# Optimization experiments

Measured on AMD Instinct MI355X. Metric: run time of the kernel, lower is better.

The kernel has to match this reference:

```python
import jax, jax.numpy as jnp
import numpy as np

B, T, V, E, U = 8192, 1, 4000, 256, 256
IN = E + E  # GRU input dim: concat(features[B,1,256], embedded tokens[B,1,256]) -> 512


def setup_inputs() -> dict:
    key = jax.random.key(0)
    ks = jax.random.split(key, 8)
    s = 0.05
    return {
        "tokens": jax.random.randint(ks[0], (B, T), 0, V),
        "features": jax.random.normal(ks[1], (B, E), jnp.float32),
        "hidden": jnp.zeros((B, U), jnp.float32),  # unused by the original call (gru gets no initial_state)
        "emb": jax.random.normal(ks[2], (V, E), jnp.float32) * s,
        "gru_kernel": jax.random.normal(ks[3], (IN, 3 * U), jnp.float32) * s,
        "gru_rkernel": jax.random.normal(ks[4], (U, 3 * U), jnp.float32) * s,
        "gru_bias": jnp.zeros((2, 3 * U), jnp.float32),  # reset_after=True: separate input/recurrent biases
        "fc1_w": jax.random.normal(ks[5], (U, U), jnp.float32) * s,
        "fc1_b": jnp.zeros((U,), jnp.float32),
        "fc2_w": jax.random.normal(ks[6], (U, V), jnp.float32) * s,
        "fc2_b": jnp.zeros((V,), jnp.float32),
    }


def reference(tokens, features, hidden, emb, gru_kernel, gru_rkernel, gru_bias,
              fc1_w, fc1_b, fc2_w, fc2_b):
    # Embedding lookup: [B,T,E]
    x = emb[tokens]
    # concat context vector on feature axis (forces T==1): [B,1,E+E]
    x = jnp.concatenate([features[:, None, :], x], axis=-1)
    # Keras GRU called without initial_state -> zeros initial state.
    h0 = jnp.zeros((x.shape[0], U), x.dtype)

    def step(h, xt):  # xt: [B, IN]; Keras GRU v3 (reset_after=True) cell; dropout off at inference
        gx = xt @ gru_kernel + gru_bias[0]      # [B, 3U]
        gh = h @ gru_rkernel + gru_bias[1]      # [B, 3U]
        xz, xr, xn = jnp.split(gx, 3, axis=-1)
        hz, hr, hn = jnp.split(gh, 3, axis=-1)
        z = jax.nn.sigmoid(xz + hz)
        r = jax.nn.sigmoid(xr + hr)
        n = jnp.tanh(xn + r * hn)
        h_new = z * h + (1.0 - z) * n
        return h_new, h_new

    state, seq = jax.lax.scan(step, h0, jnp.swapaxes(x, 0, 1))  # seq: [T,B,U]
    out = jnp.swapaxes(seq, 0, 1)               # [B,T,U]
    y = out @ fc1_w + fc1_b                     # [B,T,U]
    y = y.reshape(-1, y.shape[-1])              # [B*T, U]
    logits = y @ fc2_w + fc2_b                  # [B*T, V]
    return (logits, state)
```

## Files before the change

kernel.cpp:

```cpp
#include <hip/hip_runtime.h>
#include <stdint.h>

typedef unsigned short u16;
typedef __attribute__((ext_vector_type(8))) short bf16x8;
typedef __attribute__((ext_vector_type(4))) float f32x4;

#define Bsz   8192
#define Vv    4000
#define Vpad  4096
#define Ee    256
#define Uu    256
#define INd   512
#define G3    768

__device__ __forceinline__ u16 f2bf(float f) {
    union { float f; uint32_t i; } v; v.f = f;
    uint32_t x = v.i;
    return (u16)((x + 0x7fffu + ((x >> 16) & 1u)) >> 16);
}

__device__ __forceinline__ void gload16(const u16* g, u16* l) {
    __builtin_amdgcn_global_load_lds(
        (const __attribute__((address_space(1))) unsigned int*)g,
        (__attribute__((address_space(3))) unsigned int*)l, 16, 0, 0);
}

__global__ __launch_bounds__(256) void prep_all(
    const float* __restrict__ w1,  u16* __restrict__ w1t,
    const float* __restrict__ fc1, u16* __restrict__ fc1c,
    const float* __restrict__ fc2, u16* __restrict__ fc2t,
    const float* __restrict__ fc1b, const float* __restrict__ fc2b,
    float* __restrict__ bfused)
{
    __shared__ float t[32][33];
    __shared__ float red[4][64];
    int b = blockIdx.x;
    if (b >= 1472) {
        int nl = (b - 1472) * 64 + (threadIdx.x & 63);
        int kq = threadIdx.x >> 6;
        float s = 0.f;
        if (nl < Vv) {
            #pragma unroll 8
            for (int k = 0; k < 64; k++) {
                int kk = kq * 64 + k;
                s += fc1b[kk] * fc2[(size_t)kk * Vv + nl];
            }
        }
        red[kq][threadIdx.x & 63] = s;
        __syncthreads();
        if (kq == 0 && nl < Vv)
            bfused[nl] = red[0][nl & 63] + red[1][nl & 63] + red[2][nl & 63]
                       + red[3][nl & 63] + fc2b[nl];
        return;
    }
    if (b >= 384 && b < 448) {
        int i = (b - 384) * 1024 + threadIdx.x * 4;
        float4 v = *(const float4*)(fc1 + i);
        __align__(8) u16 o[4] = {f2bf(v.x), f2bf(v.y), f2bf(v.z), f2bf(v.w)};
        *(uint2*)&fc1c[i] = *(const uint2*)o;
        return;
    }
    const float* in; u16* out; int K, N, bx, by;
    if (b < 384) { in = w1;  out = w1t;  K = 512; N = 768; bx = b % 24;  by = b / 24; }
    else { b -= 448; in = fc2; out = fc2t; K = 256; N = Vv; bx = b % 128; by = b / 128; }
    int n0 = bx * 32, k0 = by * 32;
    int c = threadIdx.x & 31, r = threadIdx.x >> 5;
    int n = n0 + c;
    #pragma unroll
    for (int i = 0; i < 32; i += 8)
        t[r + i][c] = (n < N) ? in[(size_t)(k0 + r + i) * N + n] : 0.f;
    __syncthreads();
    #pragma unroll
    for (int i = 0; i < 32; i += 8)
        out[(size_t)(n0 + r + i) * K + k0 + c] = f2bf(t[c][r + i]);
}

__global__ __launch_bounds__(256) void gru_fused(
    const int* __restrict__ tokens, const float* __restrict__ features,
    const float* __restrict__ emb,  const u16* __restrict__ BT,
    const float* __restrict__ gb,
    u16* __restrict__ h,
    float* __restrict__ state)
{
    __shared__ __align__(16) u16 As[2][64 * 32];
    __shared__ __align__(16) u16 Bs[2][3][64 * 32];
    __shared__ int tok[64];

    int tid = threadIdx.x;
    int id  = blockIdx.y * gridDim.x + blockIdx.x;
    int sid = (id & 7) * 64 + (id >> 3);
    int m0  = (sid >> 2) * 64;
    int n0  = (sid & 3) * 64;
    if (tid < 64) tok[tid] = tokens[m0 + tid];

    int wid = tid >> 6, lane = tid & 63, quad = lane >> 4, l16 = lane & 15;
    int wm = wid * 16;

    f32x4 acc[3][4] = {};

    int r  = tid >> 2;
    int kc = (tid & 3) * 8;
    const u16* bg = BT + (size_t)(n0 + r) * INd + kc;
    const float* fsrc = features + (size_t)(m0 + r) * Ee + kc;

    #pragma unroll
    for (int g = 0; g < 3; g++)
        gload16(bg + (size_t)g * 256 * INd, &Bs[0][g][tid * 8]);
    float4 a = *(const float4*)fsrc;
    float4 c = *(const float4*)(fsrc + 4);
    {
        u16 o[8] = {f2bf(a.x), f2bf(a.y), f2bf(a.z), f2bf(a.w),
                    f2bf(c.x), f2bf(c.y), f2bf(c.z), f2bf(c.w)};
        *(uint4*)&As[0][tid * 8] = *(const uint4*)o;
    }
    a = *(const float4*)(fsrc + 32);
    c = *(const float4*)(fsrc + 36);

    int cur = 0;
    for (int k0 = 0; k0 < INd; k0 += 32) {
        __syncthreads();
        int k1 = k0 + 32;
        if (k1 < INd) {
            #pragma unroll
            for (int g = 0; g < 3; g++)
                gload16(bg + (size_t)g * 256 * INd + k1, &Bs[cur ^ 1][g][tid * 8]);
            u16 o[8] = {f2bf(a.x), f2bf(a.y), f2bf(a.z), f2bf(a.w),
                        f2bf(c.x), f2bf(c.y), f2bf(c.z), f2bf(c.w)};
            *(uint4*)&As[cur ^ 1][tid * 8] = *(const uint4*)o;
            int k2 = k0 + 64;
            if (k2 < INd) {
                const float* src = (k2 < Ee) ? (fsrc + k2)
                                 : (emb + (size_t)tok[r] * Ee + (k2 - Ee) + kc);
                a = *(const float4*)src;
                c = *(const float4*)(src + 4);
            }
        }
        bf16x8 af = *(const bf16x8*)&As[cur][(wm + l16) * 32 + quad * 8];
        #pragma unroll
        for (int g = 0; g < 3; g++)
            #pragma unroll
            for (int j = 0; j < 4; j++) {
                bf16x8 bfv = *(const bf16x8*)&Bs[cur][g][(j * 16 + l16) * 32 + quad * 8];
                acc[g][j] = __builtin_amdgcn_mfma_f32_16x16x32_bf16(af, bfv, acc[g][j], 0, 0, 0);
            }
        cur ^= 1;
    }

    #pragma unroll
    for (int j = 0; j < 4; j++) {
        int jj = n0 + j * 16 + l16;
        float bz  = gb[jj]          + gb[G3 + jj];
        float br  = gb[Uu + jj]     + gb[G3 + Uu + jj];
        float b0n = gb[2 * Uu + jj];
        float b1n = gb[G3 + 2 * Uu + jj];
        #pragma unroll
        for (int rr = 0; rr < 4; rr++) {
            int b = m0 + wm + quad * 4 + rr;
            float z  = 1.f / (1.f + __expf(-(acc[0][j][rr] + bz)));
            float rg = 1.f / (1.f + __expf(-(acc[1][j][rr] + br)));
            float n  = tanhf(acc[2][j][rr] + b0n + rg * b1n);
            float hv = (1.f - z) * n;
            h[(size_t)b * Uu + jj] = f2bf(hv);
            state[(size_t)b * Uu + jj] = hv;
        }
    }
}

template<int BMt, int BNt, bool OUT_BF16, bool HAS_BIAS>
__global__ __launch_bounds__(256) void gemm_bt(
    const u16* __restrict__ A, const u16* __restrict__ BT,
    const float* __restrict__ bias, void* __restrict__ Cout,
    int N, int K)
{
    constexpr int NW_N  = (BNt == 128) ? 2 : 1;
    constexpr int NW_M  = 4 / NW_N;
    constexpr int WROWS = BMt / NW_M;
    constexpr int MI    = WROWS / 16;

    __shared__ __align__(16) u16 As[2][BMt * 32];
    __shared__ __align__(16) u16 Bs[2][BNt * 32];

    int tid = threadIdx.x;
    int m0   = blockIdx.y * BMt;
    int n0   = blockIdx.x * BNt;
    int wid  = tid >> 6, lane = tid & 63, quad = lane >> 4, l16 = lane & 15;
    int wm   = (wid / NW_N) * WROWS;
    int wn   = (wid % NW_N) * 64;

    f32x4 acc[MI][4] = {};

    const u16* ag = A  + (size_t)(m0 + (tid >> 2)) * K + (tid & 3) * 8;
    const u16* bg = BT + (size_t)(n0 + (tid >> 2)) * K + (tid & 3) * 8;

    #pragma unroll
    for (int s = 0; s < BMt / 64; s++)
        gload16(ag + (size_t)s * 64 * K, &As[0][tid * 8 + s * 64 * 32]);
    #pragma unroll
    for (int s = 0; s < BNt / 64; s++)
        gload16(bg + (size_t)s * 64 * K, &Bs[0][tid * 8 + s * 64 * 32]);

    int cur = 0;
    for (int k0 = 0; k0 < K; k0 += 32) {
        __syncthreads();
        int k1 = k0 + 32;
        if (k1 < K) {
            #pragma unroll
            for (int s = 0; s < BMt / 64; s++)
                gload16(ag + (size_t)s * 64 * K + k1, &As[cur ^ 1][tid * 8 + s * 64 * 32]);
            #pragma unroll
            for (int s = 0; s < BNt / 64; s++)
                gload16(bg + (size_t)s * 64 * K + k1, &Bs[cur ^ 1][tid * 8 + s * 64 * 32]);
        }

        bf16x8 af[MI], bf[4];
        #pragma unroll
        for (int i = 0; i < MI; i++)
            af[i] = *(const bf16x8*)&As[cur][(wm + i * 16 + l16) * 32 + quad * 8];
        #pragma unroll
        for (int j = 0; j < 4; j++)
            bf[j] = *(const bf16x8*)&Bs[cur][(wn + j * 16 + l16) * 32 + quad * 8];
        #pragma unroll
        for (int i = 0; i < MI; i++)
            #pragma unroll
            for (int j = 0; j < 4; j++)
                acc[i][j] = __builtin_amdgcn_mfma_f32_16x16x32_bf16(af[i], bf[j], acc[i][j], 0, 0, 0);
        cur ^= 1;
    }

    #pragma unroll
    for (int i = 0; i < MI; i++)
    #pragma unroll
    for (int j = 0; j < 4; j++) {
        int gn = n0 + wn + j * 16 + l16;
        if (gn >= N) continue;
        float bv = HAS_BIAS ? bias[gn] : 0.f;
        #pragma unroll
        for (int r = 0; r < 4; r++) {
            int gm = m0 + wm + i * 16 + quad * 4 + r;
            float v = acc[i][j][r] + bv;
            if (OUT_BF16) ((u16*)Cout)[(size_t)gm * N + gn] = f2bf(v);
            else          ((float*)Cout)[(size_t)gm * N + gn] = v;
        }
    }
}

extern "C" void kernel_launch(void* const* d_in, const int* in_sizes, int n_in,
                              void* d_out, int out_size, void* d_ws, size_t ws_size,
                              hipStream_t stream)
{
    const int*   tokens   = (const int*)d_in[0];
    const float* features = (const float*)d_in[1];
    const float* emb      = (const float*)d_in[3];
    const float* w1       = (const float*)d_in[4];
    const float* gbias    = (const float*)d_in[6];
    const float* fc1w     = (const float*)d_in[7];
    const float* fc1b     = (const float*)d_in[8];
    const float* fc2w     = (const float*)d_in[9];
    const float* fc2b     = (const float*)d_in[10];

    float* logits = (float*)d_out;
    float* state  = logits + (size_t)Bsz * Vv;

    char* ws = (char*)d_ws;
    u16*   w1t    = (u16*)(ws);
    u16*   fc1c   = (u16*)(ws +   786432);
    u16*   fc2t   = (u16*)(ws +   917504);
    u16*   Wt     = (u16*)(ws +  3014656);
    u16*   h      = (u16*)(ws +  5111808);
    float* bfused = (float*)(ws + 9306112);

    prep_all<<<dim3(1536), 256, 0, stream>>>(w1, w1t, fc1w, fc1c, fc2w, fc2t,
                                             fc1b, fc2b, bfused);

    gemm_bt<64, 64, true, false><<<dim3(Uu / 64, Vpad / 64), 256, 0, stream>>>(
        fc2t, fc1c, nullptr, (void*)Wt, Uu, Uu);

    gru_fused<<<dim3(Uu / 64, Bsz / 64), 256, 0, stream>>>(
        tokens, features, emb, w1t, gbias, h, state);

    gemm_bt<128, 128, false, true><<<dim3(Vpad / 128, Bsz / 128), 256, 0, stream>>>(
        h, Wt, bfused, (void*)logits, Vv, Uu);
}
```

Measured before the change: 220.0 us.

## Merge GRU, fused-weight GEMM and bias prep into one launch

The separate prep, Wt-GEMM and GRU kernels are folded into one multi-role kernel whose block ranges run the GRU GEMM, the fc2·fc1 product, or the fused-bias reduction concurrently. The Wt product now reads fc1/fc2 in fp32 directly and converts to bf16 while staging, so the fc1 copy and fc2 transpose buffers go away. The intent is fewer launches, less intermediate global traffic, and overlap of independent work. The cost is a Wt GEMM with strided, uncoalesced fc2 loads and no async copy, plus a shared-memory footprint sized for the largest role.

Measured after the change: 211.4 us. 1.04x faster.

```diff
diff --git a/kernel.cpp b/kernel.cpp
--- a/kernel.cpp
+++ b/kernel.cpp
@@ -25,19 +25,180 @@
         (__attribute__((address_space(3))) unsigned int*)l, 16, 0, 0);
 }
 
-__global__ __launch_bounds__(256) void prep_all(
-    const float* __restrict__ w1,  u16* __restrict__ w1t,
-    const float* __restrict__ fc1, u16* __restrict__ fc1c,
-    const float* __restrict__ fc2, u16* __restrict__ fc2t,
+__global__ __launch_bounds__(256) void prep_w1(
+    const float* __restrict__ w1, u16* __restrict__ w1t)
+{
+    __shared__ float t[32][33];
+    int b  = blockIdx.x;
+    int bx = b % 24, by = b / 24;
+    int n0 = bx * 32, k0 = by * 32;
+    int c = threadIdx.x & 31, r = threadIdx.x >> 5;
+    #pragma unroll
+    for (int i = 0; i < 32; i += 8)
+        t[r + i][c] = w1[(size_t)(k0 + r + i) * 768 + n0 + c];
+    __syncthreads();
+    #pragma unroll
+    for (int i = 0; i < 32; i += 8)
+        w1t[(size_t)(n0 + r + i) * 512 + k0 + c] = f2bf(t[c][r + i]);
+}
+
+__global__ __launch_bounds__(256) void mid_all(
+    const int* __restrict__ tokens, const float* __restrict__ features,
+    const float* __restrict__ emb,  const u16* __restrict__ BT,
+    const float* __restrict__ gb,
+    u16* __restrict__ h,
+    float* __restrict__ state,
+    const float* __restrict__ fc2,
+    const float* __restrict__ fc1,
     const float* __restrict__ fc1b, const float* __restrict__ fc2b,
+    u16* __restrict__ Wt,
     float* __restrict__ bfused)
 {
-    __shared__ float t[32][33];
-    __shared__ float red[4][64];
-    int b = blockIdx.x;
-    if (b >= 1472) {
-        int nl = (b - 1472) * 64 + (threadIdx.x & 63);
-        int kq = threadIdx.x >> 6;
+    __shared__ __align__(16) char smem[33024];
+    int b   = blockIdx.x;
+    int tid = threadIdx.x;
+
+    if (b < 512) {
+        u16* AsP = (u16*)smem;
+        u16* BsP = AsP + 4096;
+        int* tok = (int*)(smem + 32768);
+
+        int sid = (b & 7) * 64 + (b >> 3);
+        int m0  = (sid >> 2) * 64;
+        int n0  = (sid & 3) * 64;
+        if (tid < 64) tok[tid] = tokens[m0 + tid];
+
+        int wid = tid >> 6, lane = tid & 63, quad = lane >> 4, l16 = lane & 15;
+        int wm = wid * 16;
+
+        f32x4 acc[3][4] = {};
+
+        int r  = tid >> 2;
+        int kc = (tid & 3) * 8;
+        const u16* bg = BT + (size_t)(n0 + r) * INd + kc;
+        const float* fsrc = features + (size_t)(m0 + r) * Ee + kc;
+
+        #pragma unroll
+        for (int g = 0; g < 3; g++)
+            gload16(bg + (size_t)g * 256 * INd, &BsP[g * 2048 + tid * 8]);
+        float4 a = *(const float4*)fsrc;
+        float4 c = *(const float4*)(fsrc + 4);
+        {
+            u16 o[8] = {f2bf(a.x), f2bf(a.y), f2bf(a.z), f2bf(a.w),
+                        f2bf(c.x), f2bf(c.y), f2bf(c.z), f2bf(c.w)};
+            *(uint4*)&AsP[tid * 8] = *(const uint4*)o;
+        }
+        a = *(const float4*)(fsrc + 32);
+        c = *(const float4*)(fsrc + 36);
+
+        int cur = 0;
+        for (int k0 = 0; k0 < INd; k0 += 32) {
+            __syncthreads();
+            int k1 = k0 + 32;
+            if (k1 < INd) {
+                #pragma unroll
+                for (int g = 0; g < 3; g++)
+                    gload16(bg + (size_t)g * 256 * INd + k1,
+                            &BsP[(cur ^ 1) * 6144 + g * 2048 + tid * 8]);
+                u16 o[8] = {f2bf(a.x), f2bf(a.y), f2bf(a.z), f2bf(a.w),
+                            f2bf(c.x), f2bf(c.y), f2bf(c.z), f2bf(c.w)};
+                *(uint4*)&AsP[(cur ^ 1) * 2048 + tid * 8] = *(const uint4*)o;
+                int k2 = k0 + 64;
+                if (k2 < INd) {
+                    const float* src = (k2 < Ee) ? (fsrc + k2)
+                                     : (emb + (size_t)tok[r] * Ee + (k2 - Ee) + kc);
+                    a = *(const float4*)src;
+                    c = *(const float4*)(src + 4);
+                }
+            }
+            bf16x8 af = *(const bf16x8*)&AsP[cur * 2048 + (wm + l16) * 32 + quad * 8];
+            #pragma unroll
+            for (int g = 0; g < 3; g++)
+                #pragma unroll
+                for (int j = 0; j < 4; j++) {
+                    bf16x8 bfv = *(const bf16x8*)&BsP[cur * 6144 + g * 2048
+                                                     + (j * 16 + l16) * 32 + quad * 8];
+                    acc[g][j] = __builtin_amdgcn_mfma_f32_16x16x32_bf16(af, bfv, acc[g][j], 0, 0, 0);
+                }
+            cur ^= 1;
+        }
+
+        #pragma unroll
+        for (int j = 0; j < 4; j++) {
+            int jj = n0 + j * 16 + l16;
+            float bz  = gb[jj]          + gb[G3 + jj];
+            float br  = gb[Uu + jj]     + gb[G3 + Uu + jj];
+            float b0n = gb[2 * Uu + jj];
+            float b1n = gb[G3 + 2 * Uu + jj];
+            #pragma unroll
+            for (int rr = 0; rr < 4; rr++) {
+                int bb = m0 + wm + quad * 4 + rr;
+                float z  = 1.f / (1.f + __expf(-(acc[0][j][rr] + bz)));
+                float rg = 1.f / (1.f + __expf(-(acc[1][j][rr] + br)));
+                float n  = tanhf(acc[2][j][rr] + b0n + rg * b1n);
+                float hv = (1.f - z) * n;
+                h[(size_t)bb * Uu + jj] = f2bf(hv);
+                state[(size_t)bb * Uu + jj] = hv;
+            }
+        }
+    } else if (b < 768) {
+        int wb = b - 512;
+        int i0 = (wb & 3) * 64;
+        int n0 = (wb >> 2) * 64;
+        u16* Aw = (u16*)smem;
+        u16* Bw = Aw + 2048;
+
+        int wid = tid >> 6, lane = tid & 63, quad = lane >> 4, l16 = lane & 15;
+        int wm  = wid * 16;
+        int nn  = tid >> 2, jc = (tid & 3) * 8;
+        int nv  = n0 + nn;
+        bool nok = nv < Vv;
+
+        f32x4 acc[4] = {};
+        float a8[8]; float4 bA, bB;
+
+        #define WT_LOAD(J0)                                                        \
+            do {                                                                   \
+                _Pragma("unroll")                                                  \
+                for (int p = 0; p < 8; p++)                                        \
+                    a8[p] = nok ? fc2[(size_t)((J0) + jc + p) * Vv + nv] : 0.f;    \
+                bA = *(const float4*)&fc1[(size_t)(i0 + nn) * 256 + (J0) + jc];    \
+                bB = *(const float4*)&fc1[(size_t)(i0 + nn) * 256 + (J0) + jc + 4];\
+            } while (0)
+
+        WT_LOAD(0);
+        for (int t = 0; t < 8; t++) {
+            __syncthreads();
+            {
+                u16 oa[8] = {f2bf(a8[0]), f2bf(a8[1]), f2bf(a8[2]), f2bf(a8[3]),
+                             f2bf(a8[4]), f2bf(a8[5]), f2bf(a8[6]), f2bf(a8[7])};
+                *(uint4*)&Aw[tid * 8] = *(const uint4*)oa;
+                u16 ob[8] = {f2bf(bA.x), f2bf(bA.y), f2bf(bA.z), f2bf(bA.w),
+                             f2bf(bB.x), f2bf(bB.y), f2bf(bB.z), f2bf(bB.w)};
+                *(uint4*)&Bw[tid * 8] = *(const uint4*)ob;
+            }
+            __syncthreads();
+            if (t < 7) WT_LOAD((t + 1) * 32);
+            bf16x8 af = *(const bf16x8*)&Aw[(wm + l16) * 32 + quad * 8];
+            #pragma unroll
+            for (int j = 0; j < 4; j++) {
+                bf16x8 bfv = *(const bf16x8*)&Bw[(j * 16 + l16) * 32 + quad * 8];
+                acc[j] = __builtin_amdgcn_mfma_f32_16x16x32_bf16(af, bfv, acc[j], 0, 0, 0);
+            }
+        }
+        #undef WT_LOAD
+
+        #pragma unroll
+        for (int j = 0; j < 4; j++)
+            #pragma unroll
+            for (int rr = 0; rr < 4; rr++)
+                Wt[(size_t)(n0 + wm + quad * 4 + rr) * 256 + i0 + j * 16 + l16]
+                    = f2bf(acc[j][rr]);
+    } else {
+        float* red = (float*)smem;
+        int bb = b - 768;
+        int nl = bb * 64 + (tid & 63);
+        int kq = tid >> 6;
         float s = 0.f;
         if (nl < Vv) {
             #pragma unroll 8
@@ -46,123 +207,11 @@
                 s += fc1b[kk] * fc2[(size_t)kk * Vv + nl];
             }
         }
-        red[kq][threadIdx.x & 63] = s;
+        red[kq * 64 + (tid & 63)] = s;
         __syncthreads();
         if (kq == 0 && nl < Vv)
-            bfused[nl] = red[0][nl & 63] + red[1][nl & 63] + red[2][nl & 63]
-                       + red[3][nl & 63] + fc2b[nl];
-        return;
-    }
-    if (b >= 384 && b < 448) {
-        int i = (b - 384) * 1024 + threadIdx.x * 4;
-        float4 v = *(const float4*)(fc1 + i);
-        __align__(8) u16 o[4] = {f2bf(v.x), f2bf(v.y), f2bf(v.z), f2bf(v.w)};
-        *(uint2*)&fc1c[i] = *(const uint2*)o;
-        return;
-    }
-    const float* in; u16* out; int K, N, bx, by;
-    if (b < 384) { in = w1;  out = w1t;  K = 512; N = 768; bx = b % 24;  by = b / 24; }
-    else { b -= 448; in = fc2; out = fc2t; K = 256; N = Vv; bx = b % 128; by = b / 128; }
-    int n0 = bx * 32, k0 = by * 32;
-    int c = threadIdx.x & 31, r = threadIdx.x >> 5;
-    int n = n0 + c;
-    #pragma unroll
-    for (int i = 0; i < 32; i += 8)
-        t[r + i][c] = (n < N) ? in[(size_t)(k0 + r + i) * N + n] : 0.f;
-    __syncthreads();
-    #pragma unroll
-    for (int i = 0; i < 32; i += 8)
-        out[(size_t)(n0 + r + i) * K + k0 + c] = f2bf(t[c][r + i]);
-}
-
-__global__ __launch_bounds__(256) void gru_fused(
-    const int* __restrict__ tokens, const float* __restrict__ features,
-    const float* __restrict__ emb,  const u16* __restrict__ BT,
-    const float* __restrict__ gb,
-    u16* __restrict__ h,
-    float* __restrict__ state)
-{
-    __shared__ __align__(16) u16 As[2][64 * 32];
-    __shared__ __align__(16) u16 Bs[2][3][64 * 32];
-    __shared__ int tok[64];
-
-    int tid = threadIdx.x;
-    int id  = blockIdx.y * gridDim.x + blockIdx.x;
-    int sid = (id & 7) * 64 + (id >> 3);
-    int m0  = (sid >> 2) * 64;
-    int n0  = (sid & 3) * 64;
-    if (tid < 64) tok[tid] = tokens[m0 + tid];
-
-    int wid = tid >> 6, lane = tid & 63, quad = lane >> 4, l16 = lane & 15;
-    int wm = wid * 16;
-
-    f32x4 acc[3][4] = {};
-
-    int r  = tid >> 2;
-    int kc = (tid & 3) * 8;
-    const u16* bg = BT + (size_t)(n0 + r) * INd + kc;
-    const float* fsrc = features + (size_t)(m0 + r) * Ee + kc;
-
-    #pragma unroll
-    for (int g = 0; g < 3; g++)
-        gload16(bg + (size_t)g * 256 * INd, &Bs[0][g][tid * 8]);
-    float4 a = *(const float4*)fsrc;
-    float4 c = *(const float4*)(fsrc + 4);
-    {
-        u16 o[8] = {f2bf(a.x), f2bf(a.y), f2bf(a.z), f2bf(a.w),
-                    f2bf(c.x), f2bf(c.y), f2bf(c.z), f2bf(c.w)};
-        *(uint4*)&As[0][tid * 8] = *(const uint4*)o;
-    }
-    a = *(const float4*)(fsrc + 32);
-    c = *(const float4*)(fsrc + 36);
-
-    int cur = 0;
-    for (int k0 = 0; k0 < INd; k0 += 32) {
-        __syncthreads();
-        int k1 = k0 + 32;
-        if (k1 < INd) {
-            #pragma unroll
-            for (int g = 0; g < 3; g++)
-                gload16(bg + (size_t)g * 256 * INd + k1, &Bs[cur ^ 1][g][tid * 8]);
-            u16 o[8] = {f2bf(a.x), f2bf(a.y), f2bf(a.z), f2bf(a.w),
-                        f2bf(c.x), f2bf(c.y), f2bf(c.z), f2bf(c.w)};
-            *(uint4*)&As[cur ^ 1][tid * 8] = *(const uint4*)o;
-            int k2 = k0 + 64;
-            if (k2 < INd) {
-                const float* src = (k2 < Ee) ? (fsrc + k2)
-                                 : (emb + (size_t)tok[r] * Ee + (k2 - Ee) + kc);
-                a = *(const float4*)src;
-                c = *(const float4*)(src + 4);
-            }
-        }
-        bf16x8 af = *(const bf16x8*)&As[cur][(wm + l16) * 32 + quad * 8];
-        #pragma unroll
-        for (int g = 0; g < 3; g++)
-            #pragma unroll
-            for (int j = 0; j < 4; j++) {
-                bf16x8 bfv = *(const bf16x8*)&Bs[cur][g][(j * 16 + l16) * 32 + quad * 8];
-                acc[g][j] = __builtin_amdgcn_mfma_f32_16x16x32_bf16(af, bfv, acc[g][j], 0, 0, 0);
-            }
-        cur ^= 1;
-    }
-
-    #pragma unroll
-    for (int j = 0; j < 4; j++) {
-        int jj = n0 + j * 16 + l16;
-        float bz  = gb[jj]          + gb[G3 + jj];
-        float br  = gb[Uu + jj]     + gb[G3 + Uu + jj];
-        float b0n = gb[2 * Uu + jj];
-        float b1n = gb[G3 + 2 * Uu + jj];
-        #pragma unroll
-        for (int rr = 0; rr < 4; rr++) {
-            int b = m0 + wm + quad * 4 + rr;
-            float z  = 1.f / (1.f + __expf(-(acc[0][j][rr] + bz)));
-            float rg = 1.f / (1.f + __expf(-(acc[1][j][rr] + br)));
-            float n  = tanhf(acc[2][j][rr] + b0n + rg * b1n);
-            float hv = (1.f - z) * n;
-            h[(size_t)b * Uu + jj] = f2bf(hv);
-            state[(size_t)b * Uu + jj] = hv;
-        }
+            bfused[nl] = red[nl & 63] + red[64 + (nl & 63)] + red[128 + (nl & 63)]
+                       + red[192 + (nl & 63)] + fc2b[nl];
     }
 }
 
@@ -263,20 +312,15 @@
 
     char* ws = (char*)d_ws;
     u16*   w1t    = (u16*)(ws);
-    u16*   fc1c   = (u16*)(ws +   786432);
-    u16*   fc2t   = (u16*)(ws +   917504);
-    u16*   Wt     = (u16*)(ws +  3014656);
-    u16*   h      = (u16*)(ws +  5111808);
-    float* bfused = (float*)(ws + 9306112);
-
-    prep_all<<<dim3(1536), 256, 0, stream>>>(w1, w1t, fc1w, fc1c, fc2w, fc2t,
-                                             fc1b, fc2b, bfused);
-
-    gemm_bt<64, 64, true, false><<<dim3(Uu / 64, Vpad / 64), 256, 0, stream>>>(
-        fc2t, fc1c, nullptr, (void*)Wt, Uu, Uu);
-
-    gru_fused<<<dim3(Uu / 64, Bsz / 64), 256, 0, stream>>>(
-        tokens, features, emb, w1t, gbias, h, state);
+    u16*   Wt     = (u16*)(ws +   786432);
+    u16*   h      = (u16*)(ws +  2883584);
+    float* bfused = (float*)(ws +  7077888);
+
+    prep_w1<<<dim3(384), 256, 0, stream>>>(w1, w1t);
+
+    mid_all<<<dim3(832), 256, 0, stream>>>(
+        tokens, features, emb, w1t, gbias, h, state,
+        fc2w, fc1w, fc1b, fc2b, Wt, bfused);
 
     gemm_bt<128, 128, false, true><<<dim3(Vpad / 128, Bsz / 128), 256, 0, stream>>>(
         h, Wt, bfused, (void*)logits, Vv, Uu);
```
